# Performance work log

Hardware: AMD Instinct MI355X
Metric: run time of the kernel (lower is better)

## Reference

```python
import jax, jax.numpy as jnp
import numpy as np

N, E, F, H, NUM_GRAPHS = 100000, 800000, 128, 64, 512


def _unif(key, shape, bound):
    return jax.random.uniform(key, shape, jnp.float32, -bound, bound)


def setup_inputs() -> dict:
    key = jax.random.key(0)
    ks = jax.random.split(key, 16)
    inp = {}
    inp["feature_matrix"] = jax.random.normal(ks[0], (N, F), jnp.float32)
    inp["edge_index"] = jax.random.randint(ks[1], (2, E), 0, N, dtype=jnp.int32)
    inp["batch"] = jnp.sort(jax.random.randint(ks[2], (N,), 0, NUM_GRAPHS, dtype=jnp.int32))
    # GraphConvolution params: uniform(-1/sqrt(out_features), ...)
    s = 1.0 / np.sqrt(H)
    inp["w1"] = _unif(ks[3], (F, H), s); inp["b1"] = _unif(ks[4], (H,), s)
    inp["w2"] = _unif(ks[5], (H, H), s); inp["b2"] = _unif(ks[6], (H,), s)
    inp["w3"] = _unif(ks[7], (H, H), s); inp["b3"] = _unif(ks[8], (H,), s)
    # Dense head params (torch Linear default: uniform(-1/sqrt(fan_in), ...)); stored as [in, out]
    s1, s2, s3 = 1.0 / np.sqrt(H), 1.0 / np.sqrt(16), 1.0 / np.sqrt(8)
    inp["dw1"] = _unif(ks[9], (H, 16), s1); inp["db1"] = _unif(ks[10], (16,), s1)
    inp["dw2"] = _unif(ks[11], (16, 8), s2); inp["db2"] = _unif(ks[12], (8,), s2)
    inp["dw3"] = _unif(ks[13], (8, 1), s3); inp["db3"] = _unif(ks[14], (1,), s3)
    return inp


def _gcn_layer(x, w, b, rows, cols, n_nodes):
    # support = X @ W ; out = A @ support where A[r, c] = 1 per edge (r, c)
    support = x @ w                                      # [N, H]
    agg = jax.ops.segment_sum(support[cols], rows, num_segments=n_nodes)
    return agg + b


def reference(feature_matrix, edge_index, batch,
              w1, b1, w2, b2, w3, b3,
              dw1, db1, dw2, db2, dw3, db3):
    n_nodes = feature_matrix.shape[0]
    rows, cols = edge_index[0], edge_index[1]
    x = jax.nn.relu(_gcn_layer(feature_matrix, w1, b1, rows, cols, n_nodes))
    x = jax.nn.relu(_gcn_layer(x, w2, b2, rows, cols, n_nodes))
    x = _gcn_layer(x, w3, b3, rows, cols, n_nodes)
    # global mean pool over graphs
    sums = jax.ops.segment_sum(x, batch, num_segments=NUM_GRAPHS)        # [G, H]
    counts = jax.ops.segment_sum(jnp.ones((n_nodes, 1), x.dtype), batch, num_segments=NUM_GRAPHS)
    x = sums / jnp.maximum(counts, 1.0)
    # MLP head
    x = jax.nn.relu(x @ dw1 + db1)
    x = jax.nn.relu(x @ dw2 + db2)
    x = jax.nn.sigmoid(x @ dw3 + db3)
    return x  # [NUM_GRAPHS, 1]
```

## Files before the change

### kernel.cpp

```cpp
#include <hip/hip_runtime.h>
#include <hip/hip_bf16.h>


static inline int divUp(int a, int b) { return (a + b - 1) / b; }

#define NXCD 8
#define CSLOT 32

using short8 = __attribute__((ext_vector_type(8))) short;
using f32x4 = __attribute__((ext_vector_type(4))) float;
using i32x4 = __attribute__((ext_vector_type(4))) int;

__device__ __forceinline__ float bf16_to_f(unsigned short h) {
    unsigned int u = ((unsigned int)h) << 16;
    return __builtin_bit_cast(float, u);
}
__device__ __forceinline__ unsigned short f_to_bf16(float f) {
    unsigned int u = __builtin_bit_cast(unsigned int, f);
    unsigned int r = (u + 0x7FFFu + ((u >> 16) & 1u)) >> 16;
    return (unsigned short)r;
}

__global__ __launch_bounds__(256) void setup_kernel(
        const float* __restrict__ w1, const float* __restrict__ w2,
        const float* __restrict__ w3, unsigned short* __restrict__ wt1,
        unsigned short* __restrict__ wt2, unsigned short* __restrict__ wt3,
        const int* __restrict__ batch, int Nn, int* __restrict__ gstart,
        int* __restrict__ gcnt, int G, int* __restrict__ fillPos, int nbBound) {
    const int b = blockIdx.x;
    const int tid = threadIdx.x;
    if (b < 3) {
        const float* W = (b == 0) ? w1 : (b == 1 ? w2 : w3);
        unsigned short* Wt = (b == 0) ? wt1 : (b == 1 ? wt2 : wt3);
        const int K = (b == 0) ? 128 : 64;
        for (int m = tid; m < 64 * K; m += 256) {
            int k = m >> 6, c = m & 63;
            Wt[c * K + k] = f_to_bf16(W[m]);
        }
    } else if (b < 3 + nbBound) {
        int g = (b - 3) * 256 + tid;
        if (g < G) {
            int lo = 0, hi = Nn;
            while (lo < hi) { int mid = (lo + hi) >> 1; if (batch[mid] < g) lo = mid + 1; else hi = mid; }
            int s = lo;
            hi = Nn;
            while (lo < hi) { int mid = (lo + hi) >> 1; if (batch[mid] < g + 1) lo = mid + 1; else hi = mid; }
            gstart[g] = s;
            gcnt[g] = lo - s;
        }
    } else {
        const int nb = gridDim.x - 3 - nbBound;
        const int cb = b - 3 - nbBound;
        const int stride = nb * 256;
        for (int i = cb * 256 + tid; i < Nn; i += stride) fillPos[i] = 0;
    }
}

template <int K>
__global__ __launch_bounds__(256) void mfma_gemm_f(const float* __restrict__ X,
                                                   const unsigned short* __restrict__ Wt,
                                                   unsigned short* __restrict__ out,
                                                   int Nrows) {
    __shared__ unsigned short Cl[64 * 72];
    const int tid = threadIdx.x;
    const int m0 = blockIdx.x * 64;
    const int lane = tid & 63;
    const int w = tid >> 6;
    const int g = lane >> 4;
    const int sl = lane & 15;
    const int r0 = w * 16;
    const int ar = m0 + r0 + sl;
    const bool aok = ar < Nrows;

    f32x4 acc[4];
#pragma unroll
    for (int cf = 0; cf < 4; ++cf) acc[cf] = (f32x4){0.f, 0.f, 0.f, 0.f};

#pragma unroll
    for (int ks = 0; ks < K / 32; ++ks) {
        const int ck = ks * 4 + g;
        short8 a = (short8){0, 0, 0, 0, 0, 0, 0, 0};
        if (aok) {
            const float* p = X + (size_t)ar * K + ck * 8;
            float4 x0 = *(const float4*)p;
            float4 x1 = *(const float4*)(p + 4);
            a[0] = (short)f_to_bf16(x0.x); a[1] = (short)f_to_bf16(x0.y);
            a[2] = (short)f_to_bf16(x0.z); a[3] = (short)f_to_bf16(x0.w);
            a[4] = (short)f_to_bf16(x1.x); a[5] = (short)f_to_bf16(x1.y);
            a[6] = (short)f_to_bf16(x1.z); a[7] = (short)f_to_bf16(x1.w);
        }
#pragma unroll
        for (int cf = 0; cf < 4; ++cf) {
            const int bc = cf * 16 + sl;
            short8 b = *(const short8*)(Wt + (size_t)bc * K + ck * 8);
            acc[cf] = __builtin_amdgcn_mfma_f32_16x16x32_bf16(a, b, acc[cf], 0, 0, 0);
        }
    }
#pragma unroll
    for (int cf = 0; cf < 4; ++cf)
#pragma unroll
        for (int rg = 0; rg < 4; ++rg) {
            int row = r0 + g * 4 + rg;
            Cl[row * 72 + cf * 16 + sl] = f_to_bf16(acc[cf][rg]);
        }
    __syncthreads();
    {
        int row = tid >> 2;
        int c0 = (tid & 3) * 16;
        int grow = m0 + row;
        if (grow < Nrows) {
            uint4 a = *(const uint4*)(Cl + row * 72 + c0);
            uint4 b = *(const uint4*)(Cl + row * 72 + c0 + 8);
            *(uint4*)(out + (size_t)grow * 64 + c0) = a;
            *(uint4*)(out + (size_t)grow * 64 + c0 + 8) = b;
        }
    }
}

__global__ __launch_bounds__(256) void fill_pad(const int* __restrict__ rows,
                                                const int* __restrict__ cols,
                                                int* __restrict__ fillPos,
                                                int* __restrict__ csrPad,
                                                int E, int Nn) {
    const int p = blockIdx.x & (NXCD - 1);
    const int lo = (int)((long)p * Nn / NXCD);
    const int hi = (int)((long)(p + 1) * Nn / NXCD);
    const int nb = gridDim.x >> 3;
    const int cb = blockIdx.x >> 3;
    const int stride4 = nb * blockDim.x * 4;
    for (int i0 = (cb * blockDim.x + threadIdx.x) * 4; i0 < E; i0 += stride4) {
        if (i0 + 3 < E) {
            i32x4 r = *(const i32x4*)(rows + i0);
            i32x4 c = *(const i32x4*)(cols + i0);
            if (r.x >= lo && r.x < hi) {
                int q = atomicAdd(&fillPos[r.x], 1);
                if (q < CSLOT) csrPad[(size_t)r.x * CSLOT + q] = c.x;
            }
            if (r.y >= lo && r.y < hi) {
                int q = atomicAdd(&fillPos[r.y], 1);
                if (q < CSLOT) csrPad[(size_t)r.y * CSLOT + q] = c.y;
            }
            if (r.z >= lo && r.z < hi) {
                int q = atomicAdd(&fillPos[r.z], 1);
                if (q < CSLOT) csrPad[(size_t)r.z * CSLOT + q] = c.z;
            }
            if (r.w >= lo && r.w < hi) {
                int q = atomicAdd(&fillPos[r.w], 1);
                if (q < CSLOT) csrPad[(size_t)r.w * CSLOT + q] = c.w;
            }
        } else {
            for (int j = i0; j < E; ++j) {
                int r = rows[j];
                if (r >= lo && r < hi) {
                    int q = atomicAdd(&fillPos[r], 1);
                    if (q < CSLOT) csrPad[(size_t)r * CSLOT + q] = cols[j];
                }
            }
        }
    }
}

__global__ __launch_bounds__(256) void fused_ag(const unsigned short* __restrict__ suppIn,
                                                const unsigned short* __restrict__ Wt,
                                                const float* __restrict__ bias,
                                                unsigned short* __restrict__ suppOut,
                                                const int* __restrict__ deg,
                                                const int* __restrict__ csrPad,
                                                int Nn) {
    __shared__ unsigned short smem[64 * 72];
    const int tid = threadIdx.x;
    const int m0 = blockIdx.x * 64;
    const int sg = tid >> 4;
    const int sl = tid & 15;
    const int laneBase = (tid & 63) & ~15;

    int d16q[4], dq[4], idxq[4];
#pragma unroll
    for (int q = 0; q < 4; ++q) {
        int node = m0 + sg + 16 * q;
        int d = (node < Nn) ? deg[node] : 0;
        d = d < CSLOT ? d : CSLOT;
        int d16 = d < 16 ? d : 16;
        dq[q] = d; d16q[q] = d16;
        idxq[q] = (sl < d16 && node < Nn) ? csrPad[(size_t)node * CSLOT + sl] : 0;
    }
    int dmax = max(max(d16q[0], d16q[1]), max(d16q[2], d16q[3]));

    float acc[4][4];
#pragma unroll
    for (int q = 0; q < 4; ++q)
#pragma unroll
        for (int k = 0; k < 4; ++k) acc[q][k] = 0.f;

    for (int i = 0; i < dmax; ++i) {
#pragma unroll
        for (int q = 0; q < 4; ++q) {
            if (i < d16q[q]) {
                int s = __shfl(idxq[q], laneBase + i);
                ushort4 v = *(const ushort4*)(suppIn + (size_t)s * 64 + sl * 4);
                acc[q][0] += bf16_to_f(v.x); acc[q][1] += bf16_to_f(v.y);
                acc[q][2] += bf16_to_f(v.z); acc[q][3] += bf16_to_f(v.w);
            }
        }
    }
#pragma unroll
    for (int q = 0; q < 4; ++q) {
        int node = m0 + sg + 16 * q;
        for (int j = 16; j < dq[q]; ++j) {
            int s = csrPad[(size_t)node * CSLOT + j];
            ushort4 v = *(const ushort4*)(suppIn + (size_t)s * 64 + sl * 4);
            acc[q][0] += bf16_to_f(v.x); acc[q][1] += bf16_to_f(v.y);
            acc[q][2] += bf16_to_f(v.z); acc[q][3] += bf16_to_f(v.w);
        }
    }
    float4 b4 = *(const float4*)(bias + sl * 4);
#pragma unroll
    for (int q = 0; q < 4; ++q) {
        int row = sg + 16 * q;
        float x0 = fmaxf(acc[q][0] + b4.x, 0.f);
        float x1 = fmaxf(acc[q][1] + b4.y, 0.f);
        float x2 = fmaxf(acc[q][2] + b4.z, 0.f);
        float x3 = fmaxf(acc[q][3] + b4.w, 0.f);
        unsigned short* dst = smem + row * 64 + (((sl >> 1) ^ (row & 7)) * 8) + (sl & 1) * 4;
        ushort4 h;
        h.x = f_to_bf16(x0); h.y = f_to_bf16(x1);
        h.z = f_to_bf16(x2); h.w = f_to_bf16(x3);
        *(ushort4*)dst = h;
    }
    __syncthreads();

    const int lane = tid & 63;
    const int w = tid >> 6;
    const int g = lane >> 4;
    const int slm = lane & 15;
    const int r0 = w * 16;
    const int arl = r0 + slm;

    f32x4 c[4];
#pragma unroll
    for (int cf = 0; cf < 4; ++cf) c[cf] = (f32x4){0.f, 0.f, 0.f, 0.f};
#pragma unroll
    for (int ks = 0; ks < 2; ++ks) {
        short8 a = *(const short8*)(smem + arl * 64 + (((ks * 4 + g) ^ (arl & 7)) * 8));
#pragma unroll
        for (int cf = 0; cf < 4; ++cf) {
            const int bc = cf * 16 + slm;
            short8 b = *(const short8*)(Wt + (size_t)bc * 64 + (ks * 4 + g) * 8);
            c[cf] = __builtin_amdgcn_mfma_f32_16x16x32_bf16(a, b, c[cf], 0, 0, 0);
        }
    }
    __syncthreads();

#pragma unroll
    for (int cf = 0; cf < 4; ++cf)
#pragma unroll
        for (int rg = 0; rg < 4; ++rg) {
            int row = r0 + g * 4 + rg;
            smem[row * 72 + cf * 16 + slm] = f_to_bf16(c[cf][rg]);
        }
    __syncthreads();
    {
        int row = tid >> 2;
        int c0 = (tid & 3) * 16;
        int grow = m0 + row;
        if (grow < Nn) {
            uint4 a = *(const uint4*)(smem + row * 72 + c0);
            uint4 b = *(const uint4*)(smem + row * 72 + c0 + 8);
            *(uint4*)(suppOut + (size_t)grow * 64 + c0) = a;
            *(uint4*)(suppOut + (size_t)grow * 64 + c0 + 8) = b;
        }
    }
}

__global__ __launch_bounds__(256) void agg64(const unsigned short* __restrict__ suppIn,
                                             const float* __restrict__ bias,
                                             unsigned short* __restrict__ out,
                                             const int* __restrict__ deg,
                                             const int* __restrict__ csrPad,
                                             int Nn) {
    const int tid = threadIdx.x;
    const int m0 = blockIdx.x * 64;
    const int sg = tid >> 4;
    const int sl = tid & 15;
    const int laneBase = (tid & 63) & ~15;

    int d16q[4], dq[4], idxq[4];
#pragma unroll
    for (int q = 0; q < 4; ++q) {
        int node = m0 + sg + 16 * q;
        int d = (node < Nn) ? deg[node] : 0;
        d = d < CSLOT ? d : CSLOT;
        int d16 = d < 16 ? d : 16;
        dq[q] = d; d16q[q] = d16;
        idxq[q] = (sl < d16 && node < Nn) ? csrPad[(size_t)node * CSLOT + sl] : 0;
    }
    int dmax = max(max(d16q[0], d16q[1]), max(d16q[2], d16q[3]));

    float acc[4][4];
#pragma unroll
    for (int q = 0; q < 4; ++q)
#pragma unroll
        for (int k = 0; k < 4; ++k) acc[q][k] = 0.f;

    for (int i = 0; i < dmax; ++i) {
#pragma unroll
        for (int q = 0; q < 4; ++q) {
            if (i < d16q[q]) {
                int s = __shfl(idxq[q], laneBase + i);
                ushort4 v = *(const ushort4*)(suppIn + (size_t)s * 64 + sl * 4);
                acc[q][0] += bf16_to_f(v.x); acc[q][1] += bf16_to_f(v.y);
                acc[q][2] += bf16_to_f(v.z); acc[q][3] += bf16_to_f(v.w);
            }
        }
    }
#pragma unroll
    for (int q = 0; q < 4; ++q) {
        int node = m0 + sg + 16 * q;
        for (int j = 16; j < dq[q]; ++j) {
            int s = csrPad[(size_t)node * CSLOT + j];
            ushort4 v = *(const ushort4*)(suppIn + (size_t)s * 64 + sl * 4);
            acc[q][0] += bf16_to_f(v.x); acc[q][1] += bf16_to_f(v.y);
            acc[q][2] += bf16_to_f(v.z); acc[q][3] += bf16_to_f(v.w);
        }
    }
    float4 b4 = *(const float4*)(bias + sl * 4);
#pragma unroll
    for (int q = 0; q < 4; ++q) {
        int node = m0 + sg + 16 * q;
        if (node >= Nn) continue;
        float x0 = acc[q][0] + b4.x, x1 = acc[q][1] + b4.y;
        float x2 = acc[q][2] + b4.z, x3 = acc[q][3] + b4.w;
        ushort4 h;
        h.x = f_to_bf16(x0); h.y = f_to_bf16(x1);
        h.z = f_to_bf16(x2); h.w = f_to_bf16(x3);
        *(ushort4*)(out + (size_t)node * 64 + sl * 4) = h;
    }
}

__global__ __launch_bounds__(256) void poolhead(const unsigned short* __restrict__ x,
                                                const int* __restrict__ gstart,
                                                const int* __restrict__ gcnt,
                                                const float* __restrict__ dw1,
                                                const float* __restrict__ db1,
                                                const float* __restrict__ dw2,
                                                const float* __restrict__ db2,
                                                const float* __restrict__ dw3,
                                                const float* __restrict__ db3,
                                                float* __restrict__ out) {
    __shared__ float red[4][64];
    __shared__ float mL[64];
    __shared__ float h1L[16];
    __shared__ float h2L[8];
    const int g = blockIdx.x;
    const int tid = threadIdx.x;
    const int lane = tid & 63;
    const int wid = tid >> 6;
    const int s = gstart[g];
    const int c = gcnt[g];

    float acc = 0.f;
    for (int i = s + wid; i < s + c; i += 4)
        acc += bf16_to_f(x[(size_t)i * 64 + lane]);
    red[wid][lane] = acc;
    __syncthreads();
    if (wid == 0)
        mL[lane] = (red[0][lane] + red[1][lane] + red[2][lane] + red[3][lane]) /
                   fmaxf((float)c, 1.f);
    __syncthreads();
    if (tid < 16) {
        float h = db1[tid];
        for (int k = 0; k < 64; ++k) h += mL[k] * dw1[k * 16 + tid];
        h1L[tid] = fmaxf(h, 0.f);
    }
    __syncthreads();
    if (tid < 8) {
        float h = db2[tid];
#pragma unroll
        for (int k = 0; k < 16; ++k) h += h1L[k] * dw2[k * 8 + tid];
        h2L[tid] = fmaxf(h, 0.f);
    }
    __syncthreads();
    if (tid == 0) {
        float z = db3[0];
#pragma unroll
        for (int k = 0; k < 8; ++k) z += h2L[k] * dw3[k];
        out[g] = 1.0f / (1.0f + expf(-z));
    }
}

extern "C" void kernel_launch(void* const* d_in, const int* in_sizes, int n_in,
                              void* d_out, int out_size, void* d_ws, size_t ws_size,
                              hipStream_t stream) {
    const float* feat = (const float*)d_in[0];
    const int* eidx   = (const int*)d_in[1];
    const int* batch  = (const int*)d_in[2];
    const float* w1 = (const float*)d_in[3];
    const float* b1 = (const float*)d_in[4];
    const float* w2 = (const float*)d_in[5];
    const float* b2 = (const float*)d_in[6];
    const float* w3 = (const float*)d_in[7];
    const float* b3 = (const float*)d_in[8];
    const float* dw1 = (const float*)d_in[9];
    const float* db1 = (const float*)d_in[10];
    const float* dw2 = (const float*)d_in[11];
    const float* db2 = (const float*)d_in[12];
    const float* dw3 = (const float*)d_in[13];
    const float* db3 = (const float*)d_in[14];

    const int H = in_sizes[4];
    const int F = in_sizes[3] / H;
    const int Nn = in_sizes[0] / F;
    const int E = in_sizes[1] / 2;
    const int G = out_size;

    const int* rows = eidx;
    const int* cols = eidx + E;

    unsigned short* supp1 = (unsigned short*)d_ws;
    unsigned short* supp2 = supp1 + (size_t)Nn * H;
    unsigned short* wt1 = supp2 + (size_t)Nn * H;
    unsigned short* wt2 = wt1 + 64 * 128;
    unsigned short* wt3 = wt2 + 64 * 64;
    int* fillPos = (int*)(wt3 + 64 * 64);
    int* csrPad = fillPos + Nn;
    int* gstart = csrPad + (size_t)Nn * CSLOT;
    int* gcnt = gstart + G;

    dim3 blk(256);
    const int gemmGrid = divUp(Nn, 64);
    const int nbBound = divUp(G, 256);

    setup_kernel<<<3 + nbBound + 56, blk, 0, stream>>>(w1, w2, w3, wt1, wt2, wt3,
                                                       batch, Nn, gstart, gcnt, G,
                                                       fillPos, nbBound);
    mfma_gemm_f<128><<<gemmGrid, blk, 0, stream>>>(feat, wt1, supp1, Nn);
    fill_pad<<<2048, blk, 0, stream>>>(rows, cols, fillPos, csrPad, E, Nn);

    fused_ag<<<gemmGrid, blk, 0, stream>>>(supp1, wt2, b1, supp2, fillPos, csrPad, Nn);
    fused_ag<<<gemmGrid, blk, 0, stream>>>(supp2, wt3, b2, supp1, fillPos, csrPad, Nn);
    agg64<<<gemmGrid, blk, 0, stream>>>(supp1, b3, supp2, fillPos, csrPad, Nn);
    poolhead<<<G, blk, 0, stream>>>(supp2, gstart, gcnt, dw1, db1, dw2, db2,
                                    dw3, db3, (float*)d_out);
}
```

Measured before the change: 194.2 us.

## Fuse first GEMM with CSR fill kernel and dual-accumulate neighbor gathers

Merges the first-layer MFMA GEMM and the padded-CSR fill into a single launch, with the two jobs given to different block ranges. The aim is to save one kernel launch and let the compute-heavy GEMM overlap with the atomic-heavy fill. It also pulls the neighbor gather into a shared helper that processes two neighbors per iteration into separate accumulators, which exposes more independent loads per thread. The extra accumulators cost registers and may lower occupancy, and the fill blocks now compete with the GEMM blocks for CUs.

```diff
diff --git a/kernel.cpp b/kernel.cpp
--- a/kernel.cpp
+++ b/kernel.cpp
@@ -56,13 +56,59 @@
     }
 }
 
-template <int K>
-__global__ __launch_bounds__(256) void mfma_gemm_f(const float* __restrict__ X,
-                                                   const unsigned short* __restrict__ Wt,
-                                                   unsigned short* __restrict__ out,
-                                                   int Nrows) {
+__global__ __launch_bounds__(256) void gemmfill(const float* __restrict__ X,
+                                                const unsigned short* __restrict__ Wt,
+                                                unsigned short* __restrict__ out,
+                                                const int* __restrict__ rows,
+                                                const int* __restrict__ cols,
+                                                int* __restrict__ fillPos,
+                                                int* __restrict__ csrPad,
+                                                int E, int Nn, int gemmBlocks) {
     __shared__ unsigned short Cl[64 * 72];
     const int tid = threadIdx.x;
+
+    if ((int)blockIdx.x >= gemmBlocks) {
+        const int fb = blockIdx.x - gemmBlocks;
+        const int nbF = (gridDim.x - gemmBlocks) >> 3;
+        const int p = fb & (NXCD - 1);
+        const int cb = fb >> 3;
+        const int lo = (int)((long)p * Nn / NXCD);
+        const int hi = (int)((long)(p + 1) * Nn / NXCD);
+        const int stride4 = nbF * 256 * 4;
+        for (int i0 = (cb * 256 + tid) * 4; i0 < E; i0 += stride4) {
+            if (i0 + 3 < E) {
+                i32x4 r = *(const i32x4*)(rows + i0);
+                i32x4 c = *(const i32x4*)(cols + i0);
+                if (r.x >= lo && r.x < hi) {
+                    int q = atomicAdd(&fillPos[r.x], 1);
+                    if (q < CSLOT) csrPad[(size_t)r.x * CSLOT + q] = c.x;
+                }
+                if (r.y >= lo && r.y < hi) {
+                    int q = atomicAdd(&fillPos[r.y], 1);
+                    if (q < CSLOT) csrPad[(size_t)r.y * CSLOT + q] = c.y;
+                }
+                if (r.z >= lo && r.z < hi) {
+                    int q = atomicAdd(&fillPos[r.z], 1);
+                    if (q < CSLOT) csrPad[(size_t)r.z * CSLOT + q] = c.z;
+                }
+                if (r.w >= lo && r.w < hi) {
+                    int q = atomicAdd(&fillPos[r.w], 1);
+                    if (q < CSLOT) csrPad[(size_t)r.w * CSLOT + q] = c.w;
+                }
+            } else {
+                for (int j = i0; j < E; ++j) {
+                    int r = rows[j];
+                    if (r >= lo && r < hi) {
+                        int q = atomicAdd(&fillPos[r], 1);
+                        if (q < CSLOT) csrPad[(size_t)r * CSLOT + q] = cols[j];
+                    }
+                }
+            }
+        }
+        return;
+    }
+
+    constexpr int K = 128;
     const int m0 = blockIdx.x * 64;
     const int lane = tid & 63;
     const int w = tid >> 6;
@@ -70,7 +116,7 @@
     const int sl = lane & 15;
     const int r0 = w * 16;
     const int ar = m0 + r0 + sl;
-    const bool aok = ar < Nrows;
+    const bool aok = ar < Nn;
 
     f32x4 acc[4];
 #pragma unroll
@@ -108,7 +154,7 @@
         int row = tid >> 2;
         int c0 = (tid & 3) * 16;
         int grow = m0 + row;
-        if (grow < Nrows) {
+        if (grow < Nn) {
             uint4 a = *(const uint4*)(Cl + row * 72 + c0);
             uint4 b = *(const uint4*)(Cl + row * 72 + c0 + 8);
             *(uint4*)(out + (size_t)grow * 64 + c0) = a;
@@ -117,46 +163,58 @@
     }
 }
 
-__global__ __launch_bounds__(256) void fill_pad(const int* __restrict__ rows,
-                                                const int* __restrict__ cols,
-                                                int* __restrict__ fillPos,
-                                                int* __restrict__ csrPad,
-                                                int E, int Nn) {
-    const int p = blockIdx.x & (NXCD - 1);
-    const int lo = (int)((long)p * Nn / NXCD);
-    const int hi = (int)((long)(p + 1) * Nn / NXCD);
-    const int nb = gridDim.x >> 3;
-    const int cb = blockIdx.x >> 3;
-    const int stride4 = nb * blockDim.x * 4;
-    for (int i0 = (cb * blockDim.x + threadIdx.x) * 4; i0 < E; i0 += stride4) {
-        if (i0 + 3 < E) {
-            i32x4 r = *(const i32x4*)(rows + i0);
-            i32x4 c = *(const i32x4*)(cols + i0);
-            if (r.x >= lo && r.x < hi) {
-                int q = atomicAdd(&fillPos[r.x], 1);
-                if (q < CSLOT) csrPad[(size_t)r.x * CSLOT + q] = c.x;
+__device__ __forceinline__ void gather4(const unsigned short* __restrict__ suppIn,
+                                        const int* __restrict__ csrPad,
+                                        const int* d16q, const int* dq,
+                                        const int* idxq, int m0, int sg, int sl,
+                                        int laneBase, float acc[4][4]) {
+    int dmax = max(max(d16q[0], d16q[1]), max(d16q[2], d16q[3]));
+    float accB[4][4];
+#pragma unroll
+    for (int q = 0; q < 4; ++q)
+#pragma unroll
+        for (int k = 0; k < 4; ++k) { acc[q][k] = 0.f; accB[q][k] = 0.f; }
+
+    int i = 0;
+    for (; i + 1 < dmax; i += 2) {
+#pragma unroll
+        for (int q = 0; q < 4; ++q) {
+            if (i < d16q[q]) {
+                int s0 = __shfl(idxq[q], laneBase + i);
+                ushort4 v0 = *(const ushort4*)(suppIn + (size_t)s0 * 64 + sl * 4);
+                acc[q][0] += bf16_to_f(v0.x); acc[q][1] += bf16_to_f(v0.y);
+                acc[q][2] += bf16_to_f(v0.z); acc[q][3] += bf16_to_f(v0.w);
             }
-            if (r.y >= lo && r.y < hi) {
-                int q = atomicAdd(&fillPos[r.y], 1);
-                if (q < CSLOT) csrPad[(size_t)r.y * CSLOT + q] = c.y;
+            if (i + 1 < d16q[q]) {
+                int s1 = __shfl(idxq[q], laneBase + i + 1);
+                ushort4 v1 = *(const ushort4*)(suppIn + (size_t)s1 * 64 + sl * 4);
+                accB[q][0] += bf16_to_f(v1.x); accB[q][1] += bf16_to_f(v1.y);
+                accB[q][2] += bf16_to_f(v1.z); accB[q][3] += bf16_to_f(v1.w);
             }
-            if (r.z >= lo && r.z < hi) {
-                int q = atomicAdd(&fillPos[r.z], 1);
-                if (q < CSLOT) csrPad[(size_t)r.z * CSLOT + q] = c.z;
+        }
+    }
+    if (i < dmax) {
+#pragma unroll
+        for (int q = 0; q < 4; ++q) {
+            if (i < d16q[q]) {
+                int s0 = __shfl(idxq[q], laneBase + i);
+                ushort4 v0 = *(const ushort4*)(suppIn + (size_t)s0 * 64 + sl * 4);
+                acc[q][0] += bf16_to_f(v0.x); acc[q][1] += bf16_to_f(v0.y);
+                acc[q][2] += bf16_to_f(v0.z); acc[q][3] += bf16_to_f(v0.w);
             }
-            if (r.w >= lo && r.w < hi) {
-                int q = atomicAdd(&fillPos[r.w], 1);
-                if (q < CSLOT) csrPad[(size_t)r.w * CSLOT + q] = c.w;
-            }
-        } else {
-            for (int j = i0; j < E; ++j) {
-                int r = rows[j];
-                if (r >= lo && r < hi) {
-                    int q = atomicAdd(&fillPos[r], 1);
-                    if (q < CSLOT) csrPad[(size_t)r * CSLOT + q] = cols[j];
-                }
-            }
-        }
+        }
+    }
+#pragma unroll
+    for (int q = 0; q < 4; ++q) {
+        int node = m0 + sg + 16 * q;
+        for (int j = 16; j < dq[q]; ++j) {
+            int s = csrPad[(size_t)node * CSLOT + j];
+            ushort4 v = *(const ushort4*)(suppIn + (size_t)s * 64 + sl * 4);
+            acc[q][0] += bf16_to_f(v.x); acc[q][1] += bf16_to_f(v.y);
+            acc[q][2] += bf16_to_f(v.z); acc[q][3] += bf16_to_f(v.w);
+        }
+#pragma unroll
+        for (int k = 0; k < 4; ++k) acc[q][k] += accB[q][k];
     }
 }
 
@@ -184,35 +242,10 @@
         dq[q] = d; d16q[q] = d16;
         idxq[q] = (sl < d16 && node < Nn) ? csrPad[(size_t)node * CSLOT + sl] : 0;
     }
-    int dmax = max(max(d16q[0], d16q[1]), max(d16q[2], d16q[3]));
 
     float acc[4][4];
-#pragma unroll
-    for (int q = 0; q < 4; ++q)
-#pragma unroll
-        for (int k = 0; k < 4; ++k) acc[q][k] = 0.f;
-
-    for (int i = 0; i < dmax; ++i) {
-#pragma unroll
-        for (int q = 0; q < 4; ++q) {
-            if (i < d16q[q]) {
-                int s = __shfl(idxq[q], laneBase + i);
-                ushort4 v = *(const ushort4*)(suppIn + (size_t)s * 64 + sl * 4);
-                acc[q][0] += bf16_to_f(v.x); acc[q][1] += bf16_to_f(v.y);
-                acc[q][2] += bf16_to_f(v.z); acc[q][3] += bf16_to_f(v.w);
-            }
-        }
-    }
-#pragma unroll
-    for (int q = 0; q < 4; ++q) {
-        int node = m0 + sg + 16 * q;
-        for (int j = 16; j < dq[q]; ++j) {
-            int s = csrPad[(size_t)node * CSLOT + j];
-            ushort4 v = *(const ushort4*)(suppIn + (size_t)s * 64 + sl * 4);
-            acc[q][0] += bf16_to_f(v.x); acc[q][1] += bf16_to_f(v.y);
-            acc[q][2] += bf16_to_f(v.z); acc[q][3] += bf16_to_f(v.w);
-        }
-    }
+    gather4(suppIn, csrPad, d16q, dq, idxq, m0, sg, sl, laneBase, acc);
+
     float4 b4 = *(const float4*)(bias + sl * 4);
 #pragma unroll
     for (int q = 0; q < 4; ++q) {
@@ -294,35 +327,10 @@
         dq[q] = d; d16q[q] = d16;
         idxq[q] = (sl < d16 && node < Nn) ? csrPad[(size_t)node * CSLOT + sl] : 0;
     }
-    int dmax = max(max(d16q[0], d16q[1]), max(d16q[2], d16q[3]));
 
     float acc[4][4];
-#pragma unroll
-    for (int q = 0; q < 4; ++q)
-#pragma unroll
-        for (int k = 0; k < 4; ++k) acc[q][k] = 0.f;
-
-    for (int i = 0; i < dmax; ++i) {
-#pragma unroll
-        for (int q = 0; q < 4; ++q) {
-            if (i < d16q[q]) {
-                int s = __shfl(idxq[q], laneBase + i);
-                ushort4 v = *(const ushort4*)(suppIn + (size_t)s * 64 + sl * 4);
-                acc[q][0] += bf16_to_f(v.x); acc[q][1] += bf16_to_f(v.y);
-                acc[q][2] += bf16_to_f(v.z); acc[q][3] += bf16_to_f(v.w);
-            }
-        }
-    }
-#pragma unroll
-    for (int q = 0; q < 4; ++q) {
-        int node = m0 + sg + 16 * q;
-        for (int j = 16; j < dq[q]; ++j) {
-            int s = csrPad[(size_t)node * CSLOT + j];
-            ushort4 v = *(const ushort4*)(suppIn + (size_t)s * 64 + sl * 4);
-            acc[q][0] += bf16_to_f(v.x); acc[q][1] += bf16_to_f(v.y);
-            acc[q][2] += bf16_to_f(v.z); acc[q][3] += bf16_to_f(v.w);
-        }
-    }
+    gather4(suppIn, csrPad, d16q, dq, idxq, m0, sg, sl, laneBase, acc);
+
     float4 b4 = *(const float4*)(bias + sl * 4);
 #pragma unroll
     for (int q = 0; q < 4; ++q) {
@@ -429,13 +437,14 @@
     dim3 blk(256);
     const int gemmGrid = divUp(Nn, 64);
     const int nbBound = divUp(G, 256);
+    const int fillBlocks = 2048;
 
     setup_kernel<<<3 + nbBound + 56, blk, 0, stream>>>(w1, w2, w3, wt1, wt2, wt3,
                                                        batch, Nn, gstart, gcnt, G,
                                                        fillPos, nbBound);
-    mfma_gemm_f<128><<<gemmGrid, blk, 0, stream>>>(feat, wt1, supp1, Nn);
-    fill_pad<<<2048, blk, 0, stream>>>(rows, cols, fillPos, csrPad, E, Nn);
-
+    gemmfill<<<gemmGrid + fillBlocks, blk, 0, stream>>>(feat, wt1, supp1,
+                                                        rows, cols, fillPos, csrPad,
+                                                        E, Nn, gemmGrid);
     fused_ag<<<gemmGrid, blk, 0, stream>>>(supp1, wt2, b1, supp2, fillPos, csrPad, Nn);
     fused_ag<<<gemmGrid, blk, 0, stream>>>(supp2, wt3, b2, supp1, fillPos, csrPad, Nn);
     agg64<<<gemmGrid, blk, 0, stream>>>(supp1, b3, supp2, fillPos, csrPad, Nn);
```

After: 212.6 us. 1.09x slower.

## Replace filtered edge scan with two-pass bucketing by XCD partition for CSR fill

Applied to the files above, without the earlier changes.

The old padded-CSR fill had every block scan all edges and keep only those whose row fell in its XCD partition, so the edge list was read eight times. The new code first buckets edges per chunk into eight partition segments using shared-memory counters, then a second kernel has each block walk its own bucket and do the fillPos atomics and csrPad writes. This cuts redundant edge reads but adds a kernel launch and an extra workspace round trip for the buckets. Bucket capacity equals chunk size, so nothing overflows.

```diff
diff --git a/kernel.cpp b/kernel.cpp
--- a/kernel.cpp
+++ b/kernel.cpp
@@ -6,6 +6,7 @@
 
 #define NXCD 8
 #define CSLOT 32
+#define NBB 512
 
 using short8 = __attribute__((ext_vector_type(8))) short;
 using f32x4 = __attribute__((ext_vector_type(4))) float;
@@ -117,46 +118,41 @@
     }
 }
 
-__global__ __launch_bounds__(256) void fill_pad(const int* __restrict__ rows,
-                                                const int* __restrict__ cols,
-                                                int* __restrict__ fillPos,
-                                                int* __restrict__ csrPad,
-                                                int E, int Nn) {
+__global__ __launch_bounds__(256) void bucket2(const int* __restrict__ rows,
+                                               const int* __restrict__ cols,
+                                               int2* __restrict__ bucket,
+                                               int* __restrict__ segCnt,
+                                               int E, int Nn, int cap, int chunk) {
+    __shared__ int cnt[NXCD];
+    const int b = blockIdx.x;
+    const int tid = threadIdx.x;
+    const int base = b * chunk;
+    const int end = min(base + chunk, E);
+    if (tid < NXCD) cnt[tid] = 0;
+    __syncthreads();
+    for (int i = base + tid; i < end; i += 256) {
+        int r = rows[i];
+        int c = cols[i];
+        int p = (int)(((long)r * NXCD) / Nn);
+        int pos = atomicAdd(&cnt[p], 1);
+        if (pos < cap) bucket[((size_t)b * NXCD + p) * cap + pos] = make_int2(r, c);
+    }
+    __syncthreads();
+    if (tid < NXCD) segCnt[b * NXCD + tid] = min(cnt[tid], cap);
+}
+
+__global__ __launch_bounds__(256) void fillB2(const int2* __restrict__ bucket,
+                                              const int* __restrict__ segCnt,
+                                              int* __restrict__ fillPos,
+                                              int* __restrict__ csrPad, int cap) {
     const int p = blockIdx.x & (NXCD - 1);
-    const int lo = (int)((long)p * Nn / NXCD);
-    const int hi = (int)((long)(p + 1) * Nn / NXCD);
-    const int nb = gridDim.x >> 3;
     const int cb = blockIdx.x >> 3;
-    const int stride4 = nb * blockDim.x * 4;
-    for (int i0 = (cb * blockDim.x + threadIdx.x) * 4; i0 < E; i0 += stride4) {
-        if (i0 + 3 < E) {
-            i32x4 r = *(const i32x4*)(rows + i0);
-            i32x4 c = *(const i32x4*)(cols + i0);
-            if (r.x >= lo && r.x < hi) {
-                int q = atomicAdd(&fillPos[r.x], 1);
-                if (q < CSLOT) csrPad[(size_t)r.x * CSLOT + q] = c.x;
-            }
-            if (r.y >= lo && r.y < hi) {
-                int q = atomicAdd(&fillPos[r.y], 1);
-                if (q < CSLOT) csrPad[(size_t)r.y * CSLOT + q] = c.y;
-            }
-            if (r.z >= lo && r.z < hi) {
-                int q = atomicAdd(&fillPos[r.z], 1);
-                if (q < CSLOT) csrPad[(size_t)r.z * CSLOT + q] = c.z;
-            }
-            if (r.w >= lo && r.w < hi) {
-                int q = atomicAdd(&fillPos[r.w], 1);
-                if (q < CSLOT) csrPad[(size_t)r.w * CSLOT + q] = c.w;
-            }
-        } else {
-            for (int j = i0; j < E; ++j) {
-                int r = rows[j];
-                if (r >= lo && r < hi) {
-                    int q = atomicAdd(&fillPos[r], 1);
-                    if (q < CSLOT) csrPad[(size_t)r * CSLOT + q] = cols[j];
-                }
-            }
-        }
+    const int cnt = segCnt[cb * NXCD + p];
+    const int2* B = bucket + ((size_t)cb * NXCD + p) * cap;
+    for (int i = threadIdx.x; i < cnt; i += 256) {
+        int2 e = B[i];
+        int q = atomicAdd(&fillPos[e.x], 1);
+        if (q < CSLOT) csrPad[(size_t)e.x * CSLOT + q] = e.y;
     }
 }
 
@@ -416,6 +412,9 @@
     const int* rows = eidx;
     const int* cols = eidx + E;
 
+    const int chunk = divUp(E, NBB);
+    const int cap = chunk;
+
     unsigned short* supp1 = (unsigned short*)d_ws;
     unsigned short* supp2 = supp1 + (size_t)Nn * H;
     unsigned short* wt1 = supp2 + (size_t)Nn * H;
@@ -425,6 +424,8 @@
     int* csrPad = fillPos + Nn;
     int* gstart = csrPad + (size_t)Nn * CSLOT;
     int* gcnt = gstart + G;
+    int* segCnt = gcnt + G;
+    int2* bucket = (int2*)(segCnt + NBB * NXCD + 2);
 
     dim3 blk(256);
     const int gemmGrid = divUp(Nn, 64);
@@ -434,7 +435,8 @@
                                                        batch, Nn, gstart, gcnt, G,
                                                        fillPos, nbBound);
     mfma_gemm_f<128><<<gemmGrid, blk, 0, stream>>>(feat, wt1, supp1, Nn);
-    fill_pad<<<2048, blk, 0, stream>>>(rows, cols, fillPos, csrPad, E, Nn);
+    bucket2<<<NBB, blk, 0, stream>>>(rows, cols, bucket, segCnt, E, Nn, cap, chunk);
+    fillB2<<<NBB * NXCD, blk, 0, stream>>>(bucket, segCnt, fillPos, csrPad, cap);
 
     fused_ag<<<gemmGrid, blk, 0, stream>>>(supp1, wt2, b1, supp2, fillPos, csrPad, Nn);
     fused_ag<<<gemmGrid, blk, 0, stream>>>(supp2, wt3, b2, supp1, fillPos, csrPad, Nn);
```

Result: no change. 194.4 us (+0.1%).
